# Kernel tuning notes

Measured on AMD Instinct MI355X. Metric: run time of the kernel, lower is better.

Reference implementation:

```python
import jax, jax.numpy as jnp
import numpy as np

L, B, S, D, H, FF, V, P = 6, 8, 1024, 768, 12, 3072, 50257, 1024
DH = D // H
EPS = 1e-5


def setup_inputs() -> dict:
    key = jax.random.key(0)
    ks = jax.random.split(key, 12)
    std = 0.02
    return {
        "x_ids": jax.random.randint(ks[0], (B, S), 0, V),
        "calibrated_mask": jax.random.normal(ks[1], (B, S, S), jnp.float32),
        "wte": jax.random.normal(ks[2], (V, D), jnp.float32) * std,
        "wpe": jax.random.normal(ks[3], (P, D), jnp.float32) * std,
        "ln1_g": jnp.ones((L, D), jnp.float32),
        "ln1_b": jnp.zeros((L, D), jnp.float32),
        "qkv_w": jax.random.normal(ks[4], (L, D, 3 * D), jnp.float32) * std,
        "qkv_b": jnp.zeros((L, 3 * D), jnp.float32),
        "ao_w": jax.random.normal(ks[5], (L, D, D), jnp.float32) * std,
        "ao_b": jnp.zeros((L, D), jnp.float32),
        "ln2_g": jnp.ones((L, D), jnp.float32),
        "ln2_b": jnp.zeros((L, D), jnp.float32),
        "fc_w": jax.random.normal(ks[6], (L, D, FF), jnp.float32) * std,
        "fc_b": jnp.zeros((L, FF), jnp.float32),
        "op_w": jax.random.normal(ks[7], (L, FF, D), jnp.float32) * std,
        "op_b": jnp.zeros((L, D), jnp.float32),
        "lnf_g": jnp.ones((D,), jnp.float32),
        "lnf_b": jnp.zeros((D,), jnp.float32),
    }


def _ln(x, g, b):
    m = jnp.mean(x, axis=-1, keepdims=True)
    v = jnp.var(x, axis=-1, keepdims=True)
    return (x - m) * jax.lax.rsqrt(v + EPS) * g + b


def _gelu_new(x):
    c = np.sqrt(2.0 / np.pi).astype(np.float32)
    return 0.5 * x * (1.0 + jnp.tanh(c * (x + 0.044715 * x * x * x)))


def _gpt2_forward(x_ids, calibrated_mask, wte, wpe, ln1_g, ln1_b, qkv_w, qkv_b,
                  ao_w, ao_b, ln2_g, ln2_b, fc_w, fc_b, op_w, op_b, lnf_g, lnf_b):
    s = x_ids.shape[1]
    h = wte[x_ids] + wpe[:s][None, :, :]  # [B,S,D]
    causal = jnp.tril(jnp.ones((s, s), bool))
    neg = jnp.finfo(h.dtype).min
    # additive mask, broadcast over heads (unsqueeze(1).repeat over n_head)
    add_mask = calibrated_mask[:, None, :, :]  # [B,1,S,S]

    def block(hid, p):
        l1g, l1b, qw, qb, aw, ab, l2g, l2b, fw, fb, ow, ob = p
        x = _ln(hid, l1g, l1b)
        qkv = x @ qw + qb  # [B,S,3D]
        q, k, v = jnp.split(qkv, 3, axis=-1)
        q = q.reshape(q.shape[0], s, H, DH).transpose(0, 2, 1, 3)
        k = k.reshape(k.shape[0], s, H, DH).transpose(0, 2, 1, 3)
        v = v.reshape(v.shape[0], s, H, DH).transpose(0, 2, 1, 3)
        scores = jnp.einsum('bhqd,bhkd->bhqk', q, k) / jnp.sqrt(jnp.asarray(DH, q.dtype))
        scores = jnp.where(causal[None, None], scores, neg)
        scores = scores + add_mask
        w = jax.nn.softmax(scores, axis=-1)
        a = jnp.einsum('bhqk,bhkd->bhqd', w, v)
        a = a.transpose(0, 2, 1, 3).reshape(a.shape[0], s, D)
        hid = hid + a @ aw + ab
        x2 = _ln(hid, l2g, l2b)
        hid = hid + _gelu_new(x2 @ fw + fb) @ ow + ob
        return hid, None

    params = (ln1_g, ln1_b, qkv_w, qkv_b, ao_w, ao_b, ln2_g, ln2_b, fc_w, fc_b, op_w, op_b)
    h, _ = jax.lax.scan(block, h, params)
    return _ln(h, lnf_g, lnf_b)


def reference(x_ids, calibrated_mask, wte, wpe, ln1_g, ln1_b, qkv_w, qkv_b,
              ao_w, ao_b, ln2_g, ln2_b, fc_w, fc_b, op_w, op_b, lnf_g, lnf_b):
    return _gpt2_forward(x_ids, calibrated_mask, wte, wpe, ln1_g, ln1_b, qkv_w, qkv_b,
                         ao_w, ao_b, ln2_g, ln2_b, fc_w, fc_b, op_w, op_b, lnf_g, lnf_b)
```

## Files before the change

kernel.cpp:

```cpp
#include <hip/hip_runtime.h>
#include <hip/hip_bf16.h>

typedef __bf16 bf16_t;
typedef __bf16 bf16x8 __attribute__((ext_vector_type(8)));
typedef float  f32x4  __attribute__((ext_vector_type(4)));

#define DEV __device__ __forceinline__

DEV void gload_lds16(const void* g, void* l) {
  __builtin_amdgcn_global_load_lds(
      (__attribute__((address_space(1))) void*)(void*)g,
      (__attribute__((address_space(3))) void*)l, 16, 0, 0);
}

__global__ __launch_bounds__(256)
void transpose_cast(const float* __restrict__ in, bf16_t* __restrict__ out,
                    int K, int N) {
  __shared__ float tile[32][33];
  const int k0 = blockIdx.x * 32;
  const int n0 = blockIdx.y * 32;
  const int tx = threadIdx.x;
  const int ty = threadIdx.y;
#pragma unroll
  for (int i = 0; i < 32; i += 8)
    tile[ty + i][tx] = in[(long)(k0 + ty + i) * N + n0 + tx];
  __syncthreads();
#pragma unroll
  for (int i = 0; i < 32; i += 8)
    out[(long)(n0 + ty + i) * K + k0 + tx] = (bf16_t)tile[tx][ty + i];
}

__global__ __launch_bounds__(256)
void embed_kernel(const int* __restrict__ ids, const float* __restrict__ wte,
                  const float* __restrict__ wpe, float* __restrict__ h) {
  const int idx = blockIdx.x * 256 + threadIdx.x;
  const int col = idx % 768;
  const int row = idx / 768;
  const int s   = row & 1023;
  h[idx] = wte[(long)ids[row] * 768 + col] + wpe[s * 768 + col];
}

template <bool BF16OUT>
__global__ __launch_bounds__(256)
void ln_kernel(const float* __restrict__ x, const float* __restrict__ g,
               const float* __restrict__ b, bf16_t* __restrict__ ob,
               float* __restrict__ of) {
  const long row = blockIdx.x;
  const float* xr = x + row * 768;
  const int t = threadIdx.x;
  float v0 = xr[t], v1 = xr[t + 256], v2 = xr[t + 512];
  float s  = v0 + v1 + v2;
  float sq = v0 * v0 + v1 * v1 + v2 * v2;
#pragma unroll
  for (int o = 32; o; o >>= 1) { s += __shfl_down(s, o); sq += __shfl_down(sq, o); }
  __shared__ float red[8];
  const int w = t >> 6;
  if ((t & 63) == 0) { red[w] = s; red[4 + w] = sq; }
  __syncthreads();
  s  = red[0] + red[1] + red[2] + red[3];
  sq = red[4] + red[5] + red[6] + red[7];
  const float mean = s * (1.f / 768.f);
  const float rs = rsqrtf(sq * (1.f / 768.f) - mean * mean + 1e-5f);
  float vv[3] = {v0, v1, v2};
#pragma unroll
  for (int i = 0; i < 3; ++i) {
    const int col = t + i * 256;
    const float o2 = (vv[i] - mean) * rs * g[col] + b[col];
    if (BF16OUT) ob[row * 768 + col] = (bf16_t)o2;
    else         of[row * 768 + col] = o2;
  }
}

template <int EPI, int BN>
__global__ __launch_bounds__(256)
void gemm_bt(const bf16_t* __restrict__ A, const bf16_t* __restrict__ Bt,
             const float* __restrict__ bias, float* __restrict__ Cf,
             bf16_t* __restrict__ Cb, int M, int N, int K) {
  constexpr int NI = BN / 32;
  __shared__ bf16_t As[2][128 * 64];
  __shared__ bf16_t Bs[2][BN * 64];
  const int tid  = threadIdx.x;
  const int lane = tid & 63, w = tid >> 6;
  const int col = lane & 15, s16 = lane >> 4;
  const int nbn = N / BN;
  const int cpx = gridDim.x >> 3;
  const int bid = (blockIdx.x & 7) * cpx + (blockIdx.x >> 3);
  const int bm = bid / nbn, bn = bid % nbn;
  const int wr = w >> 1, wc = w & 1;

  f32x4 acc[4][NI];
#pragma unroll
  for (int i = 0; i < 4; ++i)
#pragma unroll
    for (int j = 0; j < NI; ++j) acc[i][j] = f32x4{0.f, 0.f, 0.f, 0.f};

  const long arow0 = (long)bm * 128;
  const long brow0 = (long)bn * BN;

  auto stage = [&](int buf, int k0) {
#pragma unroll
    for (int i = 0; i < 4; ++i) {
      const int c = i * 256 + tid;
      const int row = c >> 3, slot = c & 7;
      gload_lds16(A + (arow0 + row) * (long)K + k0 + ((slot ^ (row & 7)) << 3),
                  (char*)&As[buf][0] + i * 4096 + w * 1024);
    }
#pragma unroll
    for (int i = 0; i < BN / 32; ++i) {
      const int c = i * 256 + tid;
      const int row = c >> 3, slot = c & 7;
      gload_lds16(Bt + (brow0 + row) * (long)K + k0 + ((slot ^ (row & 7)) << 3),
                  (char*)&Bs[buf][0] + i * 4096 + w * 1024);
    }
  };

  const int nt = K >> 6;
  stage(0, 0);
  __syncthreads();
  int cur = 0;

  for (int t = 0; t < nt; ++t) {
    if (t + 1 < nt) stage(cur ^ 1, (t + 1) << 6);

    bf16x8 af[2][4], bfr[2][NI];
#pragma unroll
    for (int mi = 0; mi < 4; ++mi) {
      const int row = wr * 64 + mi * 16 + col;
#pragma unroll
      for (int ks = 0; ks < 2; ++ks) {
        const int slot = ks * 4 + s16;
        af[ks][mi] = *(const bf16x8*)((char*)&As[cur][0] + row * 128 +
                                      ((slot ^ (row & 7)) << 4));
      }
    }
#pragma unroll
    for (int ni = 0; ni < NI; ++ni) {
      const int row = wc * (BN / 2) + ni * 16 + col;
#pragma unroll
      for (int ks = 0; ks < 2; ++ks) {
        const int slot = ks * 4 + s16;
        bfr[ks][ni] = *(const bf16x8*)((char*)&Bs[cur][0] + row * 128 +
                                       ((slot ^ (row & 7)) << 4));
      }
    }
#pragma unroll
    for (int ks = 0; ks < 2; ++ks)
#pragma unroll
      for (int mi = 0; mi < 4; ++mi)
#pragma unroll
        for (int ni = 0; ni < NI; ++ni)
          acc[mi][ni] = __builtin_amdgcn_mfma_f32_16x16x32_bf16(
              af[ks][mi], bfr[ks][ni], acc[mi][ni], 0, 0, 0);

    __syncthreads();
    cur ^= 1;
  }

  const int colb = bn * BN + wc * (BN / 2) + col;
  const int rowb = bm * 128 + wr * 64 + (s16 << 2);
#pragma unroll
  for (int ni = 0; ni < NI; ++ni) {
    const int ccol = colb + ni * 16;
    const float bv = bias[ccol];
#pragma unroll
    for (int mi = 0; mi < 4; ++mi) {
      const int row = rowb + mi * 16;
#pragma unroll
      for (int r = 0; r < 4; ++r) {
        const float v = acc[mi][ni][r] + bv;
        const long idx = (long)(row + r) * N + ccol;
        if (EPI == 0)      Cf[idx] = v;
        else if (EPI == 1) Cf[idx] += v;
        else if (EPI == 2) Cb[idx] = (bf16_t)v;
        else {
          const float z = 0.7978845608028654f * (v + 0.044715f * v * v * v);
          Cb[idx] = (bf16_t)(v / (1.f + __expf(-2.f * z)));
        }
      }
    }
  }
}

__global__ __launch_bounds__(256, 3)
void attn_kernel(const bf16_t* __restrict__ qkv, const float* __restrict__ mask,
                 bf16_t* __restrict__ out) {
  __shared__ bf16_t Kl[2][64 * 64];
  __shared__ bf16_t Vt[2][64 * 64];
  __shared__ bf16_t Pl[4][16 * 64];
  const int tid = threadIdx.x, lane = tid & 63, w = tid >> 6;
  const int col = lane & 15, s16 = lane >> 4, l7 = lane & 7;
  const int qp = blockIdx.x & 7;
  const int bh = blockIdx.x >> 3;
  const int b = bh / 12, h = bh % 12;
  const int sw0 = (s16 ^ l7) << 4;
  const int sw1 = ((s16 + 4) ^ l7) << 4;
  char* const plw = (char*)&Pl[w][0];
  const long qkvb = (long)b * 1024 * 2304;

  auto stageK = [&](int buf, int k0) {
#pragma unroll
    for (int i = 0; i < 2; ++i) {
      const int c = i * 256 + tid;
      const int krow = c >> 3, slot = c & 7;
      gload_lds16(qkv + qkvb + (long)(k0 + krow) * 2304 + 768 + h * 64 +
                      ((slot ^ (krow & 7)) << 3),
                  (char*)&Kl[buf][0] + i * 4096 + w * 1024);
    }
  };
  auto loadV = [&](int k0, bf16x8& t0, bf16x8& t1) {
    const bf16_t* vbase = qkv + qkvb + 1536 + h * 64;
#pragma unroll
    for (int i = 0; i < 2; ++i) {
      const int c = i * 256 + tid;
      const int d = c & 63, koct = c >> 6;
      const bf16_t* vsrc = vbase + (long)(k0 + koct * 8) * 2304 + d;
      bf16x8 tv;
#pragma unroll
      for (int j = 0; j < 8; ++j) tv[j] = vsrc[(long)j * 2304];
      if (i == 0) t0 = tv; else t1 = tv;
    }
  };
  auto storeV = [&](int buf, const bf16x8& t0, const bf16x8& t1) {
#pragma unroll
    for (int i = 0; i < 2; ++i) {
      const int c = i * 256 + tid;
      const int d = c & 63, koct = c >> 6;
      *(bf16x8*)((char*)&Vt[buf][0] + d * 128 + ((koct ^ (d & 7)) << 4)) =
          (i == 0) ? t0 : t1;
    }
  };

#pragma unroll 1
  for (int pass = 0; pass < 2; ++pass) {
    const int qt = pass ? (15 - qp) : qp;
    const int qrow0 = qt * 64 + w * 16;
    const long rowQ = (long)(b * 1024 + qrow0 + col) * 2304 + h * 64;
    const bf16x8 aq0 = *(const bf16x8*)&qkv[rowQ + s16 * 8];
    const bf16x8 aq1 = *(const bf16x8*)&qkv[rowQ + 32 + s16 * 8];
    const int qb = qrow0 + s16 * 4;
    const float* mrow = mask + ((long)b * 1024 + qb) * 1024;

    auto loadM = [&](int k0, float (&m)[4][4]) {
#pragma unroll
      for (int g = 0; g < 4; ++g)
#pragma unroll
        for (int r = 0; r < 4; ++r)
          m[g][r] = mrow[(long)r * 1024 + k0 + g * 16 + col];
    };

    float m_run[4], l_run[4];
    f32x4 o_acc[4];
#pragma unroll
    for (int r = 0; r < 4; ++r) { m_run[r] = -INFINITY; l_run[r] = 0.f; }
#pragma unroll
    for (int go = 0; go < 4; ++go) o_acc[go] = f32x4{0.f, 0.f, 0.f, 0.f};

    bf16x8 tv0, tv1;
    stageK(0, 0);
    loadV(0, tv0, tv1);
    storeV(0, tv0, tv1);
    float msk[4][4];
    loadM(0, msk);
    __syncthreads();

#pragma unroll 1
    for (int kt = 0; kt <= qt; ++kt) {
      const int cur = kt & 1;
      const bool more = kt < qt;
      const int k0 = kt * 64;
      float mnx[4][4];
      if (more) {
        stageK(cur ^ 1, k0 + 64);
        loadV(k0 + 64, tv0, tv1);
        loadM(k0 + 64, mnx);
      }

      f32x4 sf[4];
      __builtin_amdgcn_s_setprio(1);
#pragma unroll
      for (int g = 0; g < 4; ++g) {
        const int rbyte = (g * 16 + col) * 128;
        bf16x8 bk0 = *(const bf16x8*)((char*)&Kl[cur][0] + rbyte + sw0);
        bf16x8 bk1 = *(const bf16x8*)((char*)&Kl[cur][0] + rbyte + sw1);
        f32x4 z = f32x4{0.f, 0.f, 0.f, 0.f};
        z = __builtin_amdgcn_mfma_f32_16x16x32_bf16(aq0, bk0, z, 0, 0, 0);
        z = __builtin_amdgcn_mfma_f32_16x16x32_bf16(aq1, bk1, z, 0, 0, 0);
        sf[g] = z;
      }
      __builtin_amdgcn_s_setprio(0);

      const bool diag = (kt == qt);
      float sv[4][4];
#pragma unroll
      for (int g = 0; g < 4; ++g)
#pragma unroll
        for (int r = 0; r < 4; ++r) {
          float s = sf[g][r] * 0.125f + msk[g][r];
          if (diag && (k0 + g * 16 + col) > (qb + r)) s = -INFINITY;
          sv[g][r] = s;
        }
#pragma unroll
      for (int r = 0; r < 4; ++r) {
        float mx = fmaxf(fmaxf(sv[0][r], sv[1][r]), fmaxf(sv[2][r], sv[3][r]));
#pragma unroll
        for (int o = 8; o; o >>= 1) mx = fmaxf(mx, __shfl_xor(mx, o));
        const float m_new = fmaxf(m_run[r], mx);
        const float f = __expf(m_run[r] - m_new);
        m_run[r] = m_new;
        float sum = 0.f;
#pragma unroll
        for (int g = 0; g < 4; ++g) {
          const float p = __expf(sv[g][r] - m_new);
          sv[g][r] = p;
          sum += p;
        }
#pragma unroll
        for (int o = 8; o; o >>= 1) sum += __shfl_xor(sum, o);
        l_run[r] = l_run[r] * f + sum;
#pragma unroll
        for (int go = 0; go < 4; ++go) o_acc[go][r] *= f;
      }

#pragma unroll
      for (int g = 0; g < 4; ++g) {
        const int ks = 2 * g + (col >> 3);
#pragma unroll
        for (int r = 0; r < 4; ++r) {
          const int qr = s16 * 4 + r;
          *(bf16_t*)(plw + qr * 128 + ((ks ^ (qr & 7)) << 4) + l7 * 2) = (bf16_t)sv[g][r];
        }
      }
      const bf16x8 pa0 = *(const bf16x8*)(plw + col * 128 + sw0);
      const bf16x8 pa1 = *(const bf16x8*)(plw + col * 128 + sw1);
      __builtin_amdgcn_s_setprio(1);
#pragma unroll
      for (int go = 0; go < 4; ++go) {
        const int dbyte = (go * 16 + col) * 128;
        bf16x8 bv0 = *(const bf16x8*)((char*)&Vt[cur][0] + dbyte + sw0);
        bf16x8 bv1 = *(const bf16x8*)((char*)&Vt[cur][0] + dbyte + sw1);
        o_acc[go] = __builtin_amdgcn_mfma_f32_16x16x32_bf16(pa0, bv0, o_acc[go], 0, 0, 0);
        o_acc[go] = __builtin_amdgcn_mfma_f32_16x16x32_bf16(pa1, bv1, o_acc[go], 0, 0, 0);
      }
      __builtin_amdgcn_s_setprio(0);

      if (more) {
        storeV(cur ^ 1, tv0, tv1);
#pragma unroll
        for (int g = 0; g < 4; ++g)
#pragma unroll
          for (int r = 0; r < 4; ++r) msk[g][r] = mnx[g][r];
      }
      __syncthreads();
    }

    float inv[4];
#pragma unroll
    for (int r = 0; r < 4; ++r) inv[r] = 1.f / l_run[r];
#pragma unroll
    for (int go = 0; go < 4; ++go)
#pragma unroll
      for (int r = 0; r < 4; ++r)
        out[(long)(b * 1024 + qb + r) * 768 + h * 64 + go * 16 + col] =
            (bf16_t)(o_acc[go][r] * inv[r]);
  }
}

extern "C" void kernel_launch(void* const* d_in, const int* in_sizes, int n_in,
                              void* d_out, int out_size, void* d_ws, size_t ws_size,
                              hipStream_t stream) {
  const int*   x_ids = (const int*)d_in[0];
  const float* mask  = (const float*)d_in[1];
  const float* wte   = (const float*)d_in[2];
  const float* wpe   = (const float*)d_in[3];
  const float* ln1_g = (const float*)d_in[4];
  const float* ln1_b = (const float*)d_in[5];
  const float* qkv_w = (const float*)d_in[6];
  const float* qkv_b = (const float*)d_in[7];
  const float* ao_w  = (const float*)d_in[8];
  const float* ao_b  = (const float*)d_in[9];
  const float* ln2_g = (const float*)d_in[10];
  const float* ln2_b = (const float*)d_in[11];
  const float* fc_w  = (const float*)d_in[12];
  const float* fc_b  = (const float*)d_in[13];
  const float* op_w  = (const float*)d_in[14];
  const float* op_b  = (const float*)d_in[15];
  const float* lnf_g = (const float*)d_in[16];
  const float* lnf_b = (const float*)d_in[17];

  char* ws = (char*)d_ws;
  size_t off = 0;
  auto alloc = [&](size_t bytes) {
    char* p = ws + off;
    off += (bytes + 255) & ~(size_t)255;
    return p;
  };
  bf16_t* wqT = (bf16_t*)alloc(6ull * 2304 * 768 * 2);
  bf16_t* waT = (bf16_t*)alloc(6ull * 768 * 768 * 2);
  bf16_t* wfT = (bf16_t*)alloc(6ull * 3072 * 768 * 2);
  bf16_t* woT = (bf16_t*)alloc(6ull * 768 * 3072 * 2);
  float*  h   = (float*) alloc(8192ull * 768 * 4);
  bf16_t* xb  = (bf16_t*)alloc(8192ull * 768 * 2);
  bf16_t* qkv = (bf16_t*)alloc(8192ull * 2304 * 2);
  bf16_t* abf = (bf16_t*)alloc(8192ull * 768 * 2);
  bf16_t* fb  = (bf16_t*)alloc(8192ull * 3072 * 2);
  if (off > ws_size) return;

  const dim3 tb(32, 8);
  for (int l = 0; l < 6; ++l) {
    transpose_cast<<<dim3(768 / 32, 2304 / 32), tb, 0, stream>>>(
        qkv_w + (long)l * 768 * 2304, wqT + (long)l * 2304 * 768, 768, 2304);
    transpose_cast<<<dim3(768 / 32, 768 / 32), tb, 0, stream>>>(
        ao_w + (long)l * 768 * 768, waT + (long)l * 768 * 768, 768, 768);
    transpose_cast<<<dim3(768 / 32, 3072 / 32), tb, 0, stream>>>(
        fc_w + (long)l * 768 * 3072, wfT + (long)l * 3072 * 768, 768, 3072);
    transpose_cast<<<dim3(3072 / 32, 768 / 32), tb, 0, stream>>>(
        op_w + (long)l * 3072 * 768, woT + (long)l * 768 * 3072, 3072, 768);
  }

  embed_kernel<<<24576, 256, 0, stream>>>(x_ids, wte, wpe, h);

  for (int l = 0; l < 6; ++l) {
    ln_kernel<true><<<8192, 256, 0, stream>>>(h, ln1_g + l * 768, ln1_b + l * 768, xb, nullptr);
    gemm_bt<2, 128><<<64 * 18, 256, 0, stream>>>(xb, wqT + (long)l * 2304 * 768,
                                                 qkv_b + l * 2304, nullptr, qkv, 8192, 2304, 768);
    attn_kernel<<<768, 256, 0, stream>>>(qkv, mask, abf);
    gemm_bt<1, 64><<<64 * 12, 256, 0, stream>>>(abf, waT + (long)l * 768 * 768,
                                                ao_b + l * 768, h, nullptr, 8192, 768, 768);
    ln_kernel<true><<<8192, 256, 0, stream>>>(h, ln2_g + l * 768, ln2_b + l * 768, xb, nullptr);
    gemm_bt<3, 128><<<64 * 24, 256, 0, stream>>>(xb, wfT + (long)l * 3072 * 768,
                                                 fc_b + l * 3072, nullptr, fb, 8192, 3072, 768);
    gemm_bt<1, 64><<<64 * 12, 256, 0, stream>>>(fb, woT + (long)l * 768 * 3072,
                                                op_b + l * 768, h, nullptr, 8192, 768, 3072);
  }

  ln_kernel<false><<<8192, 256, 0, stream>>>(h, lnf_g, lnf_b, nullptr, (float*)d_out);
}
```

Baseline: 1.769 ms.

## Replace GEMM with 8-wave 128x256 tile kernel using phased ping-pong pipelining

Replaces the 4-wave gemm_bt with a 512-thread gemm8 kernel that uses 128x256 output tiles. Each K-step is split into four quadrant phases, with staged half-tile loads interleaved between barriers. The kernel uses explicit s_waitcnt, sched_barrier and s_setprio to overlap LDS reads, global-to-LDS loads and MFMA. The aim is to raise MFMA utilisation and data reuse per block. The cost is fewer blocks for the N=768 GEMMs (192) and more barriers per iteration.

```diff
diff --git a/kernel.cpp b/kernel.cpp
--- a/kernel.cpp
+++ b/kernel.cpp
@@ -12,6 +12,11 @@
       (__attribute__((address_space(1))) void*)(void*)g,
       (__attribute__((address_space(3))) void*)l, 16, 0, 0);
 }
+
+#define FENCE() asm volatile("" ::: "memory")
+#define BAR()   do { FENCE(); __builtin_amdgcn_s_barrier(); FENCE(); } while (0)
+#define LGKM0() do { asm volatile("s_waitcnt lgkmcnt(0)" ::: "memory"); \
+                     __builtin_amdgcn_sched_barrier(0); } while (0)
 
 __global__ __launch_bounds__(256)
 void transpose_cast(const float* __restrict__ in, bf16_t* __restrict__ out,
@@ -71,103 +76,158 @@
   }
 }
 
-template <int EPI, int BN>
-__global__ __launch_bounds__(256)
-void gemm_bt(const bf16_t* __restrict__ A, const bf16_t* __restrict__ Bt,
-             const float* __restrict__ bias, float* __restrict__ Cf,
-             bf16_t* __restrict__ Cb, int M, int N, int K) {
-  constexpr int NI = BN / 32;
-  __shared__ bf16_t As[2][128 * 64];
-  __shared__ bf16_t Bs[2][BN * 64];
-  const int tid  = threadIdx.x;
+template <int EPI>
+__global__ __launch_bounds__(512, 2)
+void gemm8(const bf16_t* __restrict__ A, const bf16_t* __restrict__ Bt,
+           const float* __restrict__ bias, float* __restrict__ Cf,
+           bf16_t* __restrict__ Cb, int M, int N, int K) {
+  __shared__ bf16_t As[2 * 128 * 64];
+  __shared__ bf16_t Bs[2 * 256 * 64];
+  const int tid = threadIdx.x;
   const int lane = tid & 63, w = tid >> 6;
   const int col = lane & 15, s16 = lane >> 4;
-  const int nbn = N / BN;
+  const int wm = w >> 2, wn = w & 3;
+  const int nbn = N >> 8;
   const int cpx = gridDim.x >> 3;
   const int bid = (blockIdx.x & 7) * cpx + (blockIdx.x >> 3);
   const int bm = bid / nbn, bn = bid % nbn;
-  const int wr = w >> 1, wc = w & 1;
-
-  f32x4 acc[4][NI];
+  const long arow0 = (long)bm * 128, brow0 = (long)bn * 256;
+  const int nt = K >> 6;
+
+  f32x4 acc[4][4];
 #pragma unroll
   for (int i = 0; i < 4; ++i)
 #pragma unroll
-    for (int j = 0; j < NI; ++j) acc[i][j] = f32x4{0.f, 0.f, 0.f, 0.f};
-
-  const long arow0 = (long)bm * 128;
-  const long brow0 = (long)bn * BN;
-
-  auto stage = [&](int buf, int k0) {
-#pragma unroll
-    for (int i = 0; i < 4; ++i) {
-      const int c = i * 256 + tid;
+    for (int j = 0; j < 4; ++j) acc[i][j] = f32x4{0.f, 0.f, 0.f, 0.f};
+
+  auto stageA = [&](int buf, int h, int k0) {
+    const int row = tid >> 3, slot = tid & 7;
+    gload_lds16(A + (arow0 + h * 64 + row) * (long)K + k0 + ((slot ^ (row & 7)) << 3),
+                (char*)As + buf * 16384 + h * 8192 + tid * 16);
+  };
+  auto stageB = [&](int buf, int h, int k0) {
+#pragma unroll
+    for (int i = 0; i < 2; ++i) {
+      const int c = i * 512 + tid;
       const int row = c >> 3, slot = c & 7;
-      gload_lds16(A + (arow0 + row) * (long)K + k0 + ((slot ^ (row & 7)) << 3),
-                  (char*)&As[buf][0] + i * 4096 + w * 1024);
-    }
-#pragma unroll
-    for (int i = 0; i < BN / 32; ++i) {
-      const int c = i * 256 + tid;
-      const int row = c >> 3, slot = c & 7;
-      gload_lds16(Bt + (brow0 + row) * (long)K + k0 + ((slot ^ (row & 7)) << 3),
-                  (char*)&Bs[buf][0] + i * 4096 + w * 1024);
-    }
-  };
-
-  const int nt = K >> 6;
-  stage(0, 0);
-  __syncthreads();
-  int cur = 0;
-
-  for (int t = 0; t < nt; ++t) {
-    if (t + 1 < nt) stage(cur ^ 1, (t + 1) << 6);
-
-    bf16x8 af[2][4], bfr[2][NI];
-#pragma unroll
-    for (int mi = 0; mi < 4; ++mi) {
-      const int row = wr * 64 + mi * 16 + col;
-#pragma unroll
-      for (int ks = 0; ks < 2; ++ks) {
-        const int slot = ks * 4 + s16;
-        af[ks][mi] = *(const bf16x8*)((char*)&As[cur][0] + row * 128 +
-                                      ((slot ^ (row & 7)) << 4));
-      }
-    }
-#pragma unroll
-    for (int ni = 0; ni < NI; ++ni) {
-      const int row = wc * (BN / 2) + ni * 16 + col;
-#pragma unroll
-      for (int ks = 0; ks < 2; ++ks) {
-        const int slot = ks * 4 + s16;
-        bfr[ks][ni] = *(const bf16x8*)((char*)&Bs[cur][0] + row * 128 +
-                                       ((slot ^ (row & 7)) << 4));
-      }
-    }
-#pragma unroll
-    for (int ks = 0; ks < 2; ++ks)
-#pragma unroll
-      for (int mi = 0; mi < 4; ++mi)
-#pragma unroll
-        for (int ni = 0; ni < NI; ++ni)
+      gload_lds16(Bt + (brow0 + h * 128 + row) * (long)K + k0 + ((slot ^ (row & 7)) << 3),
+                  (char*)Bs + buf * 32768 + h * 16384 + c * 16);
+    }
+  };
+  auto rdA = [&](int buf, int qm, int mi, int ks) -> bf16x8 {
+    const int lr = wm * 64 + qm * 32 + mi * 16 + col;
+    const int slot = ks * 4 + s16;
+    return *(const bf16x8*)((char*)As + buf * 16384 + lr * 128 + ((slot ^ (lr & 7)) << 4));
+  };
+  auto rdB = [&](int buf, int qn, int ni, int ks) -> bf16x8 {
+    const int lr = wn * 64 + qn * 32 + ni * 16 + col;
+    const int slot = ks * 4 + s16;
+    return *(const bf16x8*)((char*)Bs + buf * 32768 + lr * 128 + ((slot ^ (lr & 7)) << 4));
+  };
+
+  stageA(0, 0, 0);  stageA(0, 1, 0);
+  stageB(0, 0, 0);  stageB(0, 1, 0);
+  stageB(1, 0, 64); stageB(1, 1, 64);
+  asm volatile("s_waitcnt vmcnt(4)" ::: "memory");
+  BAR();
+
+  bf16x8 a0[2][2], a1[2][2], b0[2][2], b1[2][2];
+
+  for (int T = 0; T < nt; ++T) {
+    const int cur = T & 1;
+    const int kb = T << 6;
+    const bool stA = (T + 1 < nt), stB = (T + 2 < nt);
+
+#pragma unroll
+    for (int mi = 0; mi < 2; ++mi)
+#pragma unroll
+      for (int ks = 0; ks < 2; ++ks) a0[mi][ks] = rdA(cur, 0, mi, ks);
+#pragma unroll
+    for (int ni = 0; ni < 2; ++ni)
+#pragma unroll
+      for (int ks = 0; ks < 2; ++ks) b0[ni][ks] = rdB(cur, 0, ni, ks);
+    if (stA) stageA(cur ^ 1, 0, kb + 64);
+    BAR();
+    LGKM0();
+    __builtin_amdgcn_s_setprio(1);
+#pragma unroll
+    for (int mi = 0; mi < 2; ++mi)
+#pragma unroll
+      for (int ni = 0; ni < 2; ++ni)
+#pragma unroll
+        for (int ks = 0; ks < 2; ++ks)
           acc[mi][ni] = __builtin_amdgcn_mfma_f32_16x16x32_bf16(
-              af[ks][mi], bfr[ks][ni], acc[mi][ni], 0, 0, 0);
-
-    __syncthreads();
-    cur ^= 1;
-  }
-
-  const int colb = bn * BN + wc * (BN / 2) + col;
-  const int rowb = bm * 128 + wr * 64 + (s16 << 2);
-#pragma unroll
-  for (int ni = 0; ni < NI; ++ni) {
-    const int ccol = colb + ni * 16;
+              a0[mi][ks], b0[ni][ks], acc[mi][ni], 0, 0, 0);
+    __builtin_amdgcn_s_setprio(0);
+    BAR();
+
+#pragma unroll
+    for (int ni = 0; ni < 2; ++ni)
+#pragma unroll
+      for (int ks = 0; ks < 2; ++ks) b1[ni][ks] = rdB(cur, 1, ni, ks);
+    if (stA) stageA(cur ^ 1, 1, kb + 64);
+    BAR();
+    LGKM0();
+    __builtin_amdgcn_s_setprio(1);
+#pragma unroll
+    for (int mi = 0; mi < 2; ++mi)
+#pragma unroll
+      for (int ni = 0; ni < 2; ++ni)
+#pragma unroll
+        for (int ks = 0; ks < 2; ++ks)
+          acc[mi][2 + ni] = __builtin_amdgcn_mfma_f32_16x16x32_bf16(
+              a0[mi][ks], b1[ni][ks], acc[mi][2 + ni], 0, 0, 0);
+    __builtin_amdgcn_s_setprio(0);
+    BAR();
+
+#pragma unroll
+    for (int mi = 0; mi < 2; ++mi)
+#pragma unroll
+      for (int ks = 0; ks < 2; ++ks) a1[mi][ks] = rdA(cur, 1, mi, ks);
+    if (stB) stageB(cur, 0, kb + 128);
+    BAR();
+    LGKM0();
+    __builtin_amdgcn_s_setprio(1);
+#pragma unroll
+    for (int mi = 0; mi < 2; ++mi)
+#pragma unroll
+      for (int ni = 0; ni < 2; ++ni)
+#pragma unroll
+        for (int ks = 0; ks < 2; ++ks)
+          acc[2 + mi][2 + ni] = __builtin_amdgcn_mfma_f32_16x16x32_bf16(
+              a1[mi][ks], b1[ni][ks], acc[2 + mi][2 + ni], 0, 0, 0);
+    __builtin_amdgcn_s_setprio(0);
+    BAR();
+
+    if (stB) stageB(cur, 1, kb + 128);
+    if (stB) asm volatile("s_waitcnt vmcnt(4)" ::: "memory");
+    else     asm volatile("s_waitcnt vmcnt(0)" ::: "memory");
+    BAR();
+    __builtin_amdgcn_s_setprio(1);
+#pragma unroll
+    for (int mi = 0; mi < 2; ++mi)
+#pragma unroll
+      for (int ni = 0; ni < 2; ++ni)
+#pragma unroll
+        for (int ks = 0; ks < 2; ++ks)
+          acc[2 + mi][ni] = __builtin_amdgcn_mfma_f32_16x16x32_bf16(
+              a1[mi][ks], b0[ni][ks], acc[2 + mi][ni], 0, 0, 0);
+    __builtin_amdgcn_s_setprio(0);
+    BAR();
+  }
+
+  const int rowb = bm * 128 + wm * 64 + (s16 << 2);
+  const int colb = bn * 256 + wn * 64 + col;
+#pragma unroll
+  for (int n = 0; n < 4; ++n) {
+    const int ccol = colb + n * 16;
     const float bv = bias[ccol];
 #pragma unroll
-    for (int mi = 0; mi < 4; ++mi) {
-      const int row = rowb + mi * 16;
+    for (int m = 0; m < 4; ++m) {
+      const int row = rowb + m * 16;
 #pragma unroll
       for (int r = 0; r < 4; ++r) {
-        const float v = acc[mi][ni][r] + bv;
+        const float v = acc[m][n][r] + bv;
         const long idx = (long)(row + r) * N + ccol;
         if (EPI == 0)      Cf[idx] = v;
         else if (EPI == 1) Cf[idx] += v;
@@ -421,16 +481,16 @@
 
   for (int l = 0; l < 6; ++l) {
     ln_kernel<true><<<8192, 256, 0, stream>>>(h, ln1_g + l * 768, ln1_b + l * 768, xb, nullptr);
-    gemm_bt<2, 128><<<64 * 18, 256, 0, stream>>>(xb, wqT + (long)l * 2304 * 768,
-                                                 qkv_b + l * 2304, nullptr, qkv, 8192, 2304, 768);
+    gemm8<2><<<576, 512, 0, stream>>>(xb, wqT + (long)l * 2304 * 768,
+                                      qkv_b + l * 2304, nullptr, qkv, 8192, 2304, 768);
     attn_kernel<<<768, 256, 0, stream>>>(qkv, mask, abf);
-    gemm_bt<1, 64><<<64 * 12, 256, 0, stream>>>(abf, waT + (long)l * 768 * 768,
-                                                ao_b + l * 768, h, nullptr, 8192, 768, 768);
+    gemm8<1><<<192, 512, 0, stream>>>(abf, waT + (long)l * 768 * 768,
+                                      ao_b + l * 768, h, nullptr, 8192, 768, 768);
     ln_kernel<true><<<8192, 256, 0, stream>>>(h, ln2_g + l * 768, ln2_b + l * 768, xb, nullptr);
-    gemm_bt<3, 128><<<64 * 24, 256, 0, stream>>>(xb, wfT + (long)l * 3072 * 768,
-                                                 fc_b + l * 3072, nullptr, fb, 8192, 3072, 768);
-    gemm_bt<1, 64><<<64 * 12, 256, 0, stream>>>(fb, woT + (long)l * 768 * 3072,
-                                                op_b + l * 768, h, nullptr, 8192, 768, 3072);
+    gemm8<3><<<768, 512, 0, stream>>>(xb, wfT + (long)l * 3072 * 768,
+                                      fc_b + l * 3072, nullptr, fb, 8192, 3072, 768);
+    gemm8<1><<<192, 512, 0, stream>>>(fb, woT + (long)l * 768 * 3072,
+                                      op_b + l * 768, h, nullptr, 8192, 768, 3072);
   }
 
   ln_kernel<false><<<8192, 256, 0, stream>>>(h, lnf_g, lnf_b, nullptr, (float*)d_out);
```

After: 2.110 ms. 19.2% more time.

## Single-buffer GEMM LDS, raise occupancy, split-K with atomics for residual GEMMs

Applied to the files above, without the earlier changes.

The GEMM drops double-buffered LDS in favour of a single buffer with a sync after each stage, and requests four blocks per SM. Latency is then meant to be hidden by occupancy instead of software pipelining. The two residual-adding GEMMs (attention out and MLP out) switch to BN=128 with a 2-way split-K that accumulates into h via float atomicAdd, with the bias added only by the first split. Atomics make the float summation order nondeterministic and add global atomic traffic. Losing the prefetch overlap may also stall the loads.

```diff
diff --git a/kernel.cpp b/kernel.cpp
--- a/kernel.cpp
+++ b/kernel.cpp
@@ -71,22 +71,26 @@
   }
 }
 
-template <int EPI, int BN>
-__global__ __launch_bounds__(256)
+template <int EPI, int BN, int NSP>
+__global__ __launch_bounds__(256, 4)
 void gemm_bt(const bf16_t* __restrict__ A, const bf16_t* __restrict__ Bt,
              const float* __restrict__ bias, float* __restrict__ Cf,
              bf16_t* __restrict__ Cb, int M, int N, int K) {
   constexpr int NI = BN / 32;
-  __shared__ bf16_t As[2][128 * 64];
-  __shared__ bf16_t Bs[2][BN * 64];
+  __shared__ bf16_t As[128 * 64];
+  __shared__ bf16_t Bs[BN * 64];
   const int tid  = threadIdx.x;
   const int lane = tid & 63, w = tid >> 6;
   const int col = lane & 15, s16 = lane >> 4;
   const int nbn = N / BN;
   const int cpx = gridDim.x >> 3;
-  const int bid = (blockIdx.x & 7) * cpx + (blockIdx.x >> 3);
-  const int bm = bid / nbn, bn = bid % nbn;
+  const int swz = (blockIdx.x & 7) * cpx + (blockIdx.x >> 3);
+  const int ksp = (NSP > 1) ? (swz % NSP) : 0;
+  const int t0  = (NSP > 1) ? (swz / NSP) : swz;
+  const int bm = t0 / nbn, bn = t0 % nbn;
   const int wr = w >> 1, wc = w & 1;
+  const int Ksub = K / NSP;
+  const long kofs = (long)ksp * Ksub;
 
   f32x4 acc[4][NI];
 #pragma unroll
@@ -97,30 +101,27 @@
   const long arow0 = (long)bm * 128;
   const long brow0 = (long)bn * BN;
 
-  auto stage = [&](int buf, int k0) {
+  auto stage = [&](int k0) {
 #pragma unroll
     for (int i = 0; i < 4; ++i) {
       const int c = i * 256 + tid;
       const int row = c >> 3, slot = c & 7;
-      gload_lds16(A + (arow0 + row) * (long)K + k0 + ((slot ^ (row & 7)) << 3),
-                  (char*)&As[buf][0] + i * 4096 + w * 1024);
+      gload_lds16(A + (arow0 + row) * (long)K + kofs + k0 + ((slot ^ (row & 7)) << 3),
+                  (char*)As + c * 16);
     }
 #pragma unroll
     for (int i = 0; i < BN / 32; ++i) {
       const int c = i * 256 + tid;
       const int row = c >> 3, slot = c & 7;
-      gload_lds16(Bt + (brow0 + row) * (long)K + k0 + ((slot ^ (row & 7)) << 3),
-                  (char*)&Bs[buf][0] + i * 4096 + w * 1024);
+      gload_lds16(Bt + (brow0 + row) * (long)K + kofs + k0 + ((slot ^ (row & 7)) << 3),
+                  (char*)Bs + c * 16);
     }
   };
 
-  const int nt = K >> 6;
-  stage(0, 0);
-  __syncthreads();
-  int cur = 0;
-
+  const int nt = Ksub >> 6;
   for (int t = 0; t < nt; ++t) {
-    if (t + 1 < nt) stage(cur ^ 1, (t + 1) << 6);
+    stage(t << 6);
+    __syncthreads();
 
     bf16x8 af[2][4], bfr[2][NI];
 #pragma unroll
@@ -129,7 +130,7 @@
 #pragma unroll
       for (int ks = 0; ks < 2; ++ks) {
         const int slot = ks * 4 + s16;
-        af[ks][mi] = *(const bf16x8*)((char*)&As[cur][0] + row * 128 +
+        af[ks][mi] = *(const bf16x8*)((char*)As + row * 128 +
                                       ((slot ^ (row & 7)) << 4));
       }
     }
@@ -139,7 +140,7 @@
 #pragma unroll
       for (int ks = 0; ks < 2; ++ks) {
         const int slot = ks * 4 + s16;
-        bfr[ks][ni] = *(const bf16x8*)((char*)&Bs[cur][0] + row * 128 +
+        bfr[ks][ni] = *(const bf16x8*)((char*)Bs + row * 128 +
                                        ((slot ^ (row & 7)) << 4));
       }
     }
@@ -153,7 +154,6 @@
               af[ks][mi], bfr[ks][ni], acc[mi][ni], 0, 0, 0);
 
     __syncthreads();
-    cur ^= 1;
   }
 
   const int colb = bn * BN + wc * (BN / 2) + col;
@@ -161,7 +161,7 @@
 #pragma unroll
   for (int ni = 0; ni < NI; ++ni) {
     const int ccol = colb + ni * 16;
-    const float bv = bias[ccol];
+    const float bv = (EPI == 4) ? (ksp == 0 ? bias[ccol] : 0.f) : bias[ccol];
 #pragma unroll
     for (int mi = 0; mi < 4; ++mi) {
       const int row = rowb + mi * 16;
@@ -172,9 +172,11 @@
         if (EPI == 0)      Cf[idx] = v;
         else if (EPI == 1) Cf[idx] += v;
         else if (EPI == 2) Cb[idx] = (bf16_t)v;
-        else {
+        else if (EPI == 3) {
           const float z = 0.7978845608028654f * (v + 0.044715f * v * v * v);
           Cb[idx] = (bf16_t)(v / (1.f + __expf(-2.f * z)));
+        } else {
+          atomicAdd(&Cf[idx], v);
         }
       }
     }
@@ -421,15 +423,15 @@
 
   for (int l = 0; l < 6; ++l) {
     ln_kernel<true><<<8192, 256, 0, stream>>>(h, ln1_g + l * 768, ln1_b + l * 768, xb, nullptr);
-    gemm_bt<2, 128><<<64 * 18, 256, 0, stream>>>(xb, wqT + (long)l * 2304 * 768,
+    gemm_bt<2, 128, 1><<<1152, 256, 0, stream>>>(xb, wqT + (long)l * 2304 * 768,
                                                  qkv_b + l * 2304, nullptr, qkv, 8192, 2304, 768);
     attn_kernel<<<768, 256, 0, stream>>>(qkv, mask, abf);
-    gemm_bt<1, 64><<<64 * 12, 256, 0, stream>>>(abf, waT + (long)l * 768 * 768,
+    gemm_bt<4, 128, 2><<<768, 256, 0, stream>>>(abf, waT + (long)l * 768 * 768,
                                                 ao_b + l * 768, h, nullptr, 8192, 768, 768);
     ln_kernel<true><<<8192, 256, 0, stream>>>(h, ln2_g + l * 768, ln2_b + l * 768, xb, nullptr);
-    gemm_bt<3, 128><<<64 * 24, 256, 0, stream>>>(xb, wfT + (long)l * 3072 * 768,
+    gemm_bt<3, 128, 1><<<1536, 256, 0, stream>>>(xb, wfT + (long)l * 3072 * 768,
                                                  fc_b + l * 3072, nullptr, fb, 8192, 3072, 768);
-    gemm_bt<1, 64><<<64 * 12, 256, 0, stream>>>(fb, woT + (long)l * 768 * 3072,
+    gemm_bt<4, 128, 2><<<768, 256, 0, stream>>>(fb, woT + (long)l * 768 * 3072,
                                                 op_b + l * 768, h, nullptr, 8192, 768, 3072);
   }
 
```

Result: slower. 1.852 ms (+4.6%).

## Add wide 128x256 GEMM for QKV/FC and drop LDS double buffering

Applied to the files above, without the earlier changes.

Adds a 512-thread gemm_wide kernel with a 128x256 output tile, used for the QKV and FC projections to get more reuse of each A tile. Both GEMM kernels switch from a double-buffered LDS prefetch to a single buffer with sync after each load, and gemm_bt gets a min-blocks-per-CU launch bound of 4. The aim is to cut LDS footprint so more blocks fit per CU, but global-load latency is no longer overlapped with MFMA work inside a block and must be hidden by other resident blocks instead.

```diff
diff --git a/kernel.cpp b/kernel.cpp
--- a/kernel.cpp
+++ b/kernel.cpp
@@ -72,13 +72,13 @@
 }
 
 template <int EPI, int BN>
-__global__ __launch_bounds__(256)
+__global__ __launch_bounds__(256, 4)
 void gemm_bt(const bf16_t* __restrict__ A, const bf16_t* __restrict__ Bt,
              const float* __restrict__ bias, float* __restrict__ Cf,
              bf16_t* __restrict__ Cb, int M, int N, int K) {
   constexpr int NI = BN / 32;
-  __shared__ bf16_t As[2][128 * 64];
-  __shared__ bf16_t Bs[2][BN * 64];
+  __shared__ bf16_t As[128 * 64];
+  __shared__ bf16_t Bs[BN * 64];
   const int tid  = threadIdx.x;
   const int lane = tid & 63, w = tid >> 6;
   const int col = lane & 15, s16 = lane >> 4;
@@ -97,30 +97,24 @@
   const long arow0 = (long)bm * 128;
   const long brow0 = (long)bn * BN;
 
-  auto stage = [&](int buf, int k0) {
+  const int nt = K >> 6;
+  for (int t = 0; t < nt; ++t) {
+    const int k0 = t << 6;
 #pragma unroll
     for (int i = 0; i < 4; ++i) {
       const int c = i * 256 + tid;
       const int row = c >> 3, slot = c & 7;
       gload_lds16(A + (arow0 + row) * (long)K + k0 + ((slot ^ (row & 7)) << 3),
-                  (char*)&As[buf][0] + i * 4096 + w * 1024);
+                  (char*)As + c * 16);
     }
 #pragma unroll
     for (int i = 0; i < BN / 32; ++i) {
       const int c = i * 256 + tid;
       const int row = c >> 3, slot = c & 7;
       gload_lds16(Bt + (brow0 + row) * (long)K + k0 + ((slot ^ (row & 7)) << 3),
-                  (char*)&Bs[buf][0] + i * 4096 + w * 1024);
-    }
-  };
-
-  const int nt = K >> 6;
-  stage(0, 0);
-  __syncthreads();
-  int cur = 0;
-
-  for (int t = 0; t < nt; ++t) {
-    if (t + 1 < nt) stage(cur ^ 1, (t + 1) << 6);
+                  (char*)Bs + c * 16);
+    }
+    __syncthreads();
 
     bf16x8 af[2][4], bfr[2][NI];
 #pragma unroll
@@ -129,7 +123,7 @@
 #pragma unroll
       for (int ks = 0; ks < 2; ++ks) {
         const int slot = ks * 4 + s16;
-        af[ks][mi] = *(const bf16x8*)((char*)&As[cur][0] + row * 128 +
+        af[ks][mi] = *(const bf16x8*)((char*)As + row * 128 +
                                       ((slot ^ (row & 7)) << 4));
       }
     }
@@ -139,7 +133,7 @@
 #pragma unroll
       for (int ks = 0; ks < 2; ++ks) {
         const int slot = ks * 4 + s16;
-        bfr[ks][ni] = *(const bf16x8*)((char*)&Bs[cur][0] + row * 128 +
+        bfr[ks][ni] = *(const bf16x8*)((char*)Bs + row * 128 +
                                        ((slot ^ (row & 7)) << 4));
       }
     }
@@ -153,7 +147,6 @@
               af[ks][mi], bfr[ks][ni], acc[mi][ni], 0, 0, 0);
 
     __syncthreads();
-    cur ^= 1;
   }
 
   const int colb = bn * BN + wc * (BN / 2) + col;
@@ -172,6 +165,104 @@
         if (EPI == 0)      Cf[idx] = v;
         else if (EPI == 1) Cf[idx] += v;
         else if (EPI == 2) Cb[idx] = (bf16_t)v;
+        else {
+          const float z = 0.7978845608028654f * (v + 0.044715f * v * v * v);
+          Cb[idx] = (bf16_t)(v / (1.f + __expf(-2.f * z)));
+        }
+      }
+    }
+  }
+}
+
+template <int EPI>
+__global__ __launch_bounds__(512, 4)
+void gemm_wide(const bf16_t* __restrict__ A, const bf16_t* __restrict__ Bt,
+               const float* __restrict__ bias, float* __restrict__ Cf,
+               bf16_t* __restrict__ Cb, int M, int N, int K) {
+  __shared__ bf16_t As[128 * 64];
+  __shared__ bf16_t Bs[256 * 64];
+  const int tid = threadIdx.x;
+  const int lane = tid & 63, w = tid >> 6;
+  const int col = lane & 15, s16 = lane >> 4;
+  const int wm = w >> 2, wn = w & 3;
+  const int nbn = N >> 8;
+  const int cpx = gridDim.x >> 3;
+  const int bid = (blockIdx.x & 7) * cpx + (blockIdx.x >> 3);
+  const int bm = bid / nbn, bn = bid % nbn;
+  const long arow0 = (long)bm * 128, brow0 = (long)bn * 256;
+
+  f32x4 acc[4][4];
+#pragma unroll
+  for (int i = 0; i < 4; ++i)
+#pragma unroll
+    for (int j = 0; j < 4; ++j) acc[i][j] = f32x4{0.f, 0.f, 0.f, 0.f};
+
+  const int nt = K >> 6;
+  for (int t = 0; t < nt; ++t) {
+    const int k0 = t << 6;
+#pragma unroll
+    for (int i = 0; i < 2; ++i) {
+      const int c = i * 512 + tid;
+      const int row = c >> 3, slot = c & 7;
+      gload_lds16(A + (arow0 + row) * (long)K + k0 + ((slot ^ (row & 7)) << 3),
+                  (char*)As + c * 16);
+    }
+#pragma unroll
+    for (int i = 0; i < 4; ++i) {
+      const int c = i * 512 + tid;
+      const int row = c >> 3, slot = c & 7;
+      gload_lds16(Bt + (brow0 + row) * (long)K + k0 + ((slot ^ (row & 7)) << 3),
+                  (char*)Bs + c * 16);
+    }
+    __syncthreads();
+
+    bf16x8 af[2][4], bfr[2][4];
+#pragma unroll
+    for (int mi = 0; mi < 4; ++mi) {
+      const int row = wm * 64 + mi * 16 + col;
+#pragma unroll
+      for (int ks = 0; ks < 2; ++ks) {
+        const int slot = ks * 4 + s16;
+        af[ks][mi] = *(const bf16x8*)((char*)As + row * 128 +
+                                      ((slot ^ (row & 7)) << 4));
+      }
+    }
+#pragma unroll
+    for (int ni = 0; ni < 4; ++ni) {
+      const int row = wn * 64 + ni * 16 + col;
+#pragma unroll
+      for (int ks = 0; ks < 2; ++ks) {
+        const int slot = ks * 4 + s16;
+        bfr[ks][ni] = *(const bf16x8*)((char*)Bs + row * 128 +
+                                       ((slot ^ (row & 7)) << 4));
+      }
+    }
+#pragma unroll
+    for (int ks = 0; ks < 2; ++ks)
+#pragma unroll
+      for (int mi = 0; mi < 4; ++mi)
+#pragma unroll
+        for (int ni = 0; ni < 4; ++ni)
+          acc[mi][ni] = __builtin_amdgcn_mfma_f32_16x16x32_bf16(
+              af[ks][mi], bfr[ks][ni], acc[mi][ni], 0, 0, 0);
+
+    __syncthreads();
+  }
+
+  const int rowb = bm * 128 + wm * 64 + (s16 << 2);
+  const int colb = bn * 256 + wn * 64 + col;
+#pragma unroll
+  for (int ni = 0; ni < 4; ++ni) {
+    const int ccol = colb + ni * 16;
+    const float bv = bias[ccol];
+#pragma unroll
+    for (int mi = 0; mi < 4; ++mi) {
+      const int row = rowb + mi * 16;
+#pragma unroll
+      for (int r = 0; r < 4; ++r) {
+        const float v = acc[mi][ni][r] + bv;
+        const long idx = (long)(row + r) * N + ccol;
+        if (EPI == 2) Cb[idx] = (bf16_t)v;
         else {
           const float z = 0.7978845608028654f * (v + 0.044715f * v * v * v);
           Cb[idx] = (bf16_t)(v / (1.f + __expf(-2.f * z)));
@@ -421,16 +512,16 @@
 
   for (int l = 0; l < 6; ++l) {
     ln_kernel<true><<<8192, 256, 0, stream>>>(h, ln1_g + l * 768, ln1_b + l * 768, xb, nullptr);
-    gemm_bt<2, 128><<<64 * 18, 256, 0, stream>>>(xb, wqT + (long)l * 2304 * 768,
-                                                 qkv_b + l * 2304, nullptr, qkv, 8192, 2304, 768);
+    gemm_wide<2><<<576, 512, 0, stream>>>(xb, wqT + (long)l * 2304 * 768,
+                                          qkv_b + l * 2304, nullptr, qkv, 8192, 2304, 768);
     attn_kernel<<<768, 256, 0, stream>>>(qkv, mask, abf);
-    gemm_bt<1, 64><<<64 * 12, 256, 0, stream>>>(abf, waT + (long)l * 768 * 768,
-                                                ao_b + l * 768, h, nullptr, 8192, 768, 768);
+    gemm_bt<1, 64><<<768, 256, 0, stream>>>(abf, waT + (long)l * 768 * 768,
+                                            ao_b + l * 768, h, nullptr, 8192, 768, 768);
     ln_kernel<true><<<8192, 256, 0, stream>>>(h, ln2_g + l * 768, ln2_b + l * 768, xb, nullptr);
-    gemm_bt<3, 128><<<64 * 24, 256, 0, stream>>>(xb, wfT + (long)l * 3072 * 768,
-                                                 fc_b + l * 3072, nullptr, fb, 8192, 3072, 768);
-    gemm_bt<1, 64><<<64 * 12, 256, 0, stream>>>(fb, woT + (long)l * 768 * 3072,
-                                                op_b + l * 768, h, nullptr, 8192, 768, 3072);
+    gemm_wide<3><<<768, 512, 0, stream>>>(xb, wfT + (long)l * 3072 * 768,
+                                          fc_b + l * 3072, nullptr, fb, 8192, 3072, 768);
+    gemm_bt<1, 64><<<768, 256, 0, stream>>>(fb, woT + (long)l * 768 * 3072,
+                                            op_b + l * 768, h, nullptr, 8192, 768, 3072);
   }
 
   ln_kernel<false><<<8192, 256, 0, stream>>>(h, lnf_g, lnf_b, nullptr, (float*)d_out);
```

Result: no change. 1.738 ms (-1.8%).
